# Kernel optimization log

Hardware: AMD Instinct MI355X
Metric: run time of the kernel (lower is better)

## Reference

```python
import jax, jax.numpy as jnp
import numpy as np

N_NODES = 100000
N_EDGES = 1600000
F_IN, F_HID, F_OUT = 48, 16, 16
K = 2  # kernel_size, dim=1, degree=1 open B-spline -> basis (1-u, u)


def glorot(key, shape):
    fan_in, fan_out = shape[-2], shape[-1]
    s = jnp.sqrt(6.0 / (fan_in + fan_out))
    return jax.random.uniform(key, shape, jnp.float32, -s, s)


def setup_inputs() -> dict:
    key = jax.random.key(0)
    ks = jax.random.split(key, 10)
    x = jax.random.normal(ks[0], (N_NODES, F_IN), jnp.float32)
    edge_attr = jax.random.uniform(ks[1], (N_EDGES, 1), jnp.float32)
    edge_index = jax.random.randint(ks[2], (2, N_EDGES), 0, N_NODES, jnp.int64)
    W1 = glorot(ks[3], (K, F_IN, F_HID))
    root1 = glorot(ks[4], (F_IN, F_HID))
    b1 = jnp.zeros((F_HID,), jnp.float32)
    W2 = glorot(ks[5], (K, F_HID, F_OUT))
    root2 = glorot(ks[6], (F_HID, F_OUT))
    b2 = jnp.zeros((F_OUT,), jnp.float32)
    return {"x": x, "edge_attr": edge_attr, "edge_index": edge_index,
            "W1": W1, "root1": root1, "b1": b1, "W2": W2, "root2": root2, "b2": b2}


def spline_conv(x, edge_index, u, W, root, bias, num_nodes):
    # x: [N,Fin], u: [E] pseudo coords in [0,1], W: [2,Fin,Fout]
    src, dst = edge_index[0], edge_index[1]
    xj = x[src]                                        # [E,Fin] gather
    m = jnp.einsum('ef,kfo->eko', xj, W)               # [E,2,Fout]
    basis = jnp.stack([1.0 - u, u], axis=1)            # linear open B-spline, K=2
    msg = jnp.einsum('ek,eko->eo', basis, m)           # [E,Fout]
    agg = jax.ops.segment_sum(msg, dst, num_segments=num_nodes)
    cnt = jax.ops.segment_sum(jnp.ones_like(msg[:, 0]), dst, num_segments=num_nodes)
    agg = agg / jnp.maximum(cnt, 1.0)[:, None]         # aggr='mean'
    return agg + x @ root + bias                       # root_weight + bias


def reference(x, edge_attr, edge_index, W1, root1, b1, W2, root2, b2):
    u = edge_attr[:, 0]
    h = jax.nn.elu(spline_conv(x, edge_index, u, W1, root1, b1, N_NODES))
    out = spline_conv(h, edge_index, u, W2, root2, b2, N_NODES)
    return jax.nn.log_softmax(out, axis=1)
```

## Files before the change

kernel.cpp:

```cpp
#include <hip/hip_runtime.h>
#include <math.h>

#define N_NODES 100000
#define N_EDGES 1600000
#define KC 8
#define KSH 3
#define NBUK 391
#define NCHUNK 256
#define CPE 6250
#define M_CNT (NBUK * NCHUNK)
#define SCB 512
#define NSC ((M_CNT + SCB - 1) / SCB)

__device__ __forceinline__ unsigned bf16_rne(float x) {
    unsigned u = __float_as_uint(x);
    return (u + 0x7FFFu + ((u >> 16) & 1u)) >> 16;
}

__device__ __forceinline__ void acc4(float* acc, uint4 w, float uu) {
    acc[0] += fmaf(uu, __uint_as_float(w.x & 0xFFFF0000u), __uint_as_float(w.x << 16));
    acc[1] += fmaf(uu, __uint_as_float(w.y & 0xFFFF0000u), __uint_as_float(w.y << 16));
    acc[2] += fmaf(uu, __uint_as_float(w.z & 0xFFFF0000u), __uint_as_float(w.z << 16));
    acc[3] += fmaf(uu, __uint_as_float(w.w & 0xFFFF0000u), __uint_as_float(w.w << 16));
}

__device__ __forceinline__ void edge_accum(unsigned pk,
                                           const uint4* __restrict__ YPH,
                                           float acc[16]) {
    float uu = (float)(pk >> 17) * (1.0f / 32767.0f);
    const uint4* yp = YPH + (size_t)(pk & 0x1FFFFu) * 4;
    uint4 w0 = yp[0], w1 = yp[1], w2 = yp[2], w3 = yp[3];
    acc4(acc + 0, w0, uu);
    acc4(acc + 4, w1, uu);
    acc4(acc + 8, w2, uu);
    acc4(acc + 12, w3, uu);
}

__device__ __forceinline__ void edge_accum2(unsigned p0, unsigned p1,
                                            const uint4* __restrict__ YPH,
                                            float acc[16]) {
    float u0 = (float)(p0 >> 17) * (1.0f / 32767.0f);
    float u1 = (float)(p1 >> 17) * (1.0f / 32767.0f);
    const uint4* a = YPH + (size_t)(p0 & 0x1FFFFu) * 4;
    const uint4* b = YPH + (size_t)(p1 & 0x1FFFFu) * 4;
    uint4 w0 = a[0], w1 = a[1], w2 = a[2], w3 = a[3];
    uint4 v0 = b[0], v1 = b[1], v2 = b[2], v3 = b[3];
    acc4(acc + 0, w0, u0);
    acc4(acc + 4, w1, u0);
    acc4(acc + 8, w2, u0);
    acc4(acc + 12, w3, u0);
    acc4(acc + 0, v0, u1);
    acc4(acc + 4, v1, u1);
    acc4(acc + 8, v2, u1);
    acc4(acc + 12, v3, u1);
}

__global__ __launch_bounds__(1024)
void fused_hist_transform(const float* __restrict__ X,
                          const float* __restrict__ W,
                          const float* __restrict__ root,
                          const float* __restrict__ bias,
                          unsigned* __restrict__ YPH, float* __restrict__ R,
                          const int* __restrict__ dst,
                          int* __restrict__ counts) {
    int t = threadIdx.x;
    if (blockIdx.x < NCHUNK) {
        __shared__ int h[NBUK];
        for (int i = t; i < NBUK; i += 1024) h[i] = 0;
        __syncthreads();
        int c = blockIdx.x;
        const int* dp = dst + c * CPE;
        for (int j = t; j < CPE; j += 1024) atomicAdd(&h[dp[j] >> 8], 1);
        __syncthreads();
        for (int i = t; i < NBUK; i += 1024) counts[i * NCHUNK + c] = h[i];
    } else {
        __shared__ float sW0[48 * 16];
        __shared__ float sWd[48 * 16];
        __shared__ float sR[48 * 16];
        __shared__ float sB[16];
        int bid = blockIdx.x - NCHUNK;
        for (int i = t; i < 48 * 16; i += 1024) {
            float w0 = W[i];
            float w1 = W[48 * 16 + i];
            sW0[i] = w0;
            sWd[i] = w1 - w0;
            sR[i]  = root[i];
        }
        if (t < 16) sB[t] = bias[t];
        __syncthreads();

        int idx = bid * 1024 + t;
        int n = idx >> 4;
        int o = idx & 15;
        if (n >= N_NODES) return;

        const float* xr = X + (long)n * 48;
        float a0 = 0.0f, a1 = 0.0f, ar = 0.0f;
        for (int f = 0; f < 48; ++f) {
            float xv = xr[f];
            a0 = fmaf(xv, sW0[f * 16 + o], a0);
            a1 = fmaf(xv, sWd[f * 16 + o], a1);
            ar = fmaf(xv, sR[f * 16 + o], ar);
        }
        YPH[idx] = bf16_rne(a0) | (bf16_rne(a1) << 16);
        R[idx]   = ar + sB[o];
    }
}

__global__ __launch_bounds__(SCB)
void scan_blocksum(const int* __restrict__ a, int* __restrict__ bsum) {
    __shared__ int s[SCB];
    int t = threadIdx.x;
    int i = blockIdx.x * SCB + t;
    s[t] = (i < M_CNT) ? a[i] : 0;
    __syncthreads();
    for (int off = SCB / 2; off > 0; off >>= 1) {
        if (t < off) s[t] += s[t + off];
        __syncthreads();
    }
    if (t == 0) bsum[blockIdx.x] = s[0];
}

__global__ __launch_bounds__(256)
void scan_bsum(int* __restrict__ bsum) {
    __shared__ int s[256];
    int t = threadIdx.x;
    int v = (t < NSC) ? bsum[t] : 0;
    s[t] = v;
    __syncthreads();
    for (int off = 1; off < 256; off <<= 1) {
        int x = (t >= off) ? s[t - off] : 0;
        __syncthreads();
        s[t] += x;
        __syncthreads();
    }
    if (t < NSC) bsum[t] = s[t] - v;
}

__global__ __launch_bounds__(SCB)
void scan_write(int* __restrict__ a, const int* __restrict__ bsum) {
    __shared__ int s[SCB];
    int t = threadIdx.x;
    int i = blockIdx.x * SCB + t;
    int v = (i < M_CNT) ? a[i] : 0;
    s[t] = v;
    __syncthreads();
    for (int off = 1; off < SCB; off <<= 1) {
        int x = (t >= off) ? s[t - off] : 0;
        __syncthreads();
        s[t] += x;
        __syncthreads();
    }
    if (i < M_CNT) a[i] = bsum[blockIdx.x] + s[t] - v;
}

__global__ __launch_bounds__(1024)
void scatter_edges(const int* __restrict__ src, const int* __restrict__ dst,
                   const float* __restrict__ u,
                   const int* __restrict__ offsets,
                   unsigned* __restrict__ pk, unsigned char* __restrict__ dl) {
    __shared__ unsigned upk[CPE];
    __shared__ unsigned short ubuk[CPE];
    __shared__ unsigned char udl[CPE];
    __shared__ unsigned spk[CPE];
    __shared__ unsigned char sdl[CPE];
    __shared__ int ls[NBUK + 1];
    __shared__ int lcur[NBUK];
    __shared__ int gbase[NBUK];
    __shared__ int sc[SCB];

    int t = threadIdx.x, c = blockIdx.x;

    for (int i = t; i < NBUK; i += 1024) lcur[i] = 0;
    __syncthreads();
    for (int j = t; j < CPE; j += 1024) {
        int e = c * CPE + j;
        int d = dst[e];
        float uu = u[e];
        uu = uu < 0.0f ? 0.0f : (uu > 1.0f ? 1.0f : uu);
        int u15 = (int)fmaf(uu, 32767.0f, 0.5f);
        upk[j] = (unsigned)src[e] | ((unsigned)u15 << 17);
        udl[j] = (unsigned char)(d & 255);
        int b = d >> 8;
        ubuk[j] = (unsigned short)b;
        atomicAdd(&lcur[b], 1);
    }
    __syncthreads();

    int v = 0;
    if (t < SCB) {
        v = (t < NBUK) ? lcur[t] : 0;
        sc[t] = v;
    }
    __syncthreads();
    for (int off = 1; off < SCB; off <<= 1) {
        int x = 0;
        if (t < SCB && t >= off) x = sc[t - off];
        __syncthreads();
        if (t < SCB) sc[t] += x;
        __syncthreads();
    }
    if (t < NBUK) {
        int ex = sc[t] - v;
        ls[t] = ex;
        lcur[t] = ex;
        gbase[t] = offsets[t * NCHUNK + c] - ex;
    }
    if (t == 0) ls[NBUK] = CPE;
    __syncthreads();

    for (int j = t; j < CPE; j += 1024) {
        int b = ubuk[j];
        int p = atomicAdd(&lcur[b], 1);
        spk[p] = upk[j];
        sdl[p] = udl[j];
    }
    __syncthreads();

    for (int j = t; j < CPE; j += 1024) {
        int lo = 0, hi = NBUK;
        while (hi - lo > 1) {
            int mid = (lo + hi) >> 1;
            if (ls[mid] <= j) lo = mid; else hi = mid;
        }
        int g = gbase[lo] + j;
        pk[g] = spk[j];
        dl[g] = sdl[j];
    }
}

__global__ __launch_bounds__(256)
void group_edges(const int* __restrict__ offsets,
                 const unsigned* __restrict__ pk_in,
                 const unsigned char* __restrict__ dl,
                 unsigned* __restrict__ pk_out,
                 int* __restrict__ rowptr) {
    __shared__ int h[256];
    __shared__ int pre[256];
    int b = blockIdx.x, t = threadIdx.x;
    int beg = offsets[b * NCHUNK];
    int end = (b + 1 < NBUK) ? offsets[(b + 1) * NCHUNK] : N_EDGES;
    h[t] = 0;
    __syncthreads();
    for (int j = beg + t; j < end; j += 256) atomicAdd(&h[dl[j]], 1);
    __syncthreads();
    int cntv = h[t];
    pre[t] = cntv;
    __syncthreads();
    for (int off = 1; off < 256; off <<= 1) {
        int x = (t >= off) ? pre[t - off] : 0;
        __syncthreads();
        pre[t] += x;
        __syncthreads();
    }
    int ex = pre[t] - cntv;
    int node0 = b << 8;
    if (node0 + t < N_NODES) rowptr[node0 + t] = beg + ex;
    if (b == 0 && t == 0) rowptr[N_NODES] = N_EDGES;
    __syncthreads();
    h[t] = ex;
    __syncthreads();
    for (int j = beg + t; j < end; j += 256) {
        int loc = dl[j];
        int pos = atomicAdd(&h[loc], 1);
        pk_out[beg + pos] = pk_in[j];
    }
}

__global__ __launch_bounds__(256)
void aggregate_elu_transform(const int* __restrict__ rowptr,
                             const unsigned* __restrict__ csr,
                             const uint4* __restrict__ YPH1,
                             const float* __restrict__ R1,
                             const float* __restrict__ W2,
                             const float* __restrict__ root2,
                             const float* __restrict__ b2,
                             unsigned* __restrict__ YPH2,
                             float* __restrict__ R2) {
    __shared__ float sW0[16 * 16];
    __shared__ float sWd[16 * 16];
    __shared__ float sR[16 * 16];
    __shared__ float sB[16];
    int t = threadIdx.x;
    {
        float w0 = W2[t];
        float w1 = W2[256 + t];
        sW0[t] = w0;
        sWd[t] = w1 - w0;
        sR[t]  = root2[t];
    }
    if (t < 16) sB[t] = b2[t];
    __syncthreads();

    int g = blockIdx.x * 256 + t;
    int n = g >> KSH;
    int h = g & (KC - 1);
    int beg = rowptr[n], end = rowptr[n + 1];
    int deg = end - beg;

    float acc[16];
#pragma unroll
    for (int i = 0; i < 16; ++i) acc[i] = 0.0f;
    int j = beg + h;
    for (; j + KC < end; j += 2 * KC) edge_accum2(csr[j], csr[j + KC], YPH1, acc);
    if (j < end) edge_accum(csr[j], YPH1, acc);

#pragma unroll
    for (int mask = 1; mask <= 4; mask <<= 1) {
#pragma unroll
        for (int i = 0; i < 16; ++i) acc[i] += __shfl_xor(acc[i], mask);
    }
    float inv = 1.0f / (deg > 0 ? (float)deg : 1.0f);

    float h16[16];
    const float4* rp = (const float4*)(R1 + (size_t)n * 16);
#pragma unroll
    for (int q = 0; q < 4; ++q) {
        float4 rr = rp[q];
        float v;
        v = fmaf(acc[4 * q + 0], inv, rr.x); h16[4 * q + 0] = v > 0.0f ? v : expm1f(v);
        v = fmaf(acc[4 * q + 1], inv, rr.y); h16[4 * q + 1] = v > 0.0f ? v : expm1f(v);
        v = fmaf(acc[4 * q + 2], inv, rr.z); h16[4 * q + 2] = v > 0.0f ? v : expm1f(v);
        v = fmaf(acc[4 * q + 3], inv, rr.w); h16[4 * q + 3] = v > 0.0f ? v : expm1f(v);
    }

    int o0 = 2 * h;
    float a0 = 0.0f, a1 = 0.0f, ar = 0.0f;
    float c0 = 0.0f, c1 = 0.0f, cr = 0.0f;
#pragma unroll
    for (int f = 0; f < 16; ++f) {
        float hv = h16[f];
        a0 = fmaf(hv, sW0[f * 16 + o0], a0);
        a1 = fmaf(hv, sWd[f * 16 + o0], a1);
        ar = fmaf(hv, sR[f * 16 + o0],  ar);
        c0 = fmaf(hv, sW0[f * 16 + o0 + 1], c0);
        c1 = fmaf(hv, sWd[f * 16 + o0 + 1], c1);
        cr = fmaf(hv, sR[f * 16 + o0 + 1],  cr);
    }
    ((uint2*)YPH2)[g] = make_uint2(bf16_rne(a0) | (bf16_rne(a1) << 16),
                                   bf16_rne(c0) | (bf16_rne(c1) << 16));
    ((float2*)R2)[g] = make_float2(ar + sB[o0], cr + sB[o0 + 1]);
}

__global__ __launch_bounds__(256)
void aggregate_logsoftmax(const int* __restrict__ rowptr,
                          const unsigned* __restrict__ csr,
                          const uint4* __restrict__ YPH,
                          const float* __restrict__ R,
                          float* __restrict__ out) {
    int g = blockIdx.x * 256 + threadIdx.x;
    int n = g >> KSH;
    int h = g & (KC - 1);
    int beg = rowptr[n], end = rowptr[n + 1];
    int deg = end - beg;

    float acc[16];
#pragma unroll
    for (int i = 0; i < 16; ++i) acc[i] = 0.0f;
    int j = beg + h;
    for (; j + KC < end; j += 2 * KC) edge_accum2(csr[j], csr[j + KC], YPH, acc);
    if (j < end) edge_accum(csr[j], YPH, acc);

#pragma unroll
    for (int mask = 1; mask <= 4; mask <<= 1) {
#pragma unroll
        for (int i = 0; i < 16; ++i) acc[i] += __shfl_xor(acc[i], mask);
    }
    float inv = 1.0f / (deg > 0 ? (float)deg : 1.0f);

    float2 rr = ((const float2*)R)[g];
    float v0 = fmaf(acc[2 * h + 0], inv, rr.x);
    float v1 = fmaf(acc[2 * h + 1], inv, rr.y);

    float m = fmaxf(v0, v1);
#pragma unroll
    for (int mask = 1; mask <= 4; mask <<= 1) m = fmaxf(m, __shfl_xor(m, mask));
    float s = expf(v0 - m) + expf(v1 - m);
#pragma unroll
    for (int mask = 1; mask <= 4; mask <<= 1) s += __shfl_xor(s, mask);
    float lse = m + logf(s);

    ((float2*)out)[g] = make_float2(v0 - lse, v1 - lse);
}

extern "C" void kernel_launch(void* const* d_in, const int* in_sizes, int n_in,
                              void* d_out, int out_size, void* d_ws, size_t ws_size,
                              hipStream_t stream) {
    const float* x         = (const float*)d_in[0];
    const float* edge_attr = (const float*)d_in[1];
    const int*   edge_idx  = (const int*)d_in[2];
    const float* W1        = (const float*)d_in[3];
    const float* root1     = (const float*)d_in[4];
    const float* b1        = (const float*)d_in[5];
    const float* W2        = (const float*)d_in[6];
    const float* root2     = (const float*)d_in[7];
    const float* b2        = (const float*)d_in[8];
    float* out = (float*)d_out;

    const int* src = edge_idx;
    const int* dst = edge_idx + N_EDGES;

    char* ws = (char*)d_ws;
    unsigned*      pk_in   = (unsigned*)(ws);
    unsigned*      pk_out  = (unsigned*)(ws + 6400000);
    unsigned char* dl      = (unsigned char*)(ws + 12800000);
    int*           counts  = (int*)(ws + 14400000);
    int*           rowptr  = (int*)(ws + 14800384);
    unsigned*      YPH1    = (unsigned*)(ws + 15200400);
    unsigned*      YPH2    = (unsigned*)(ws + 21600400);
    float*         R1      = (float*)(ws + 28000400);
    float*         R2      = (float*)(ws + 34400400);
    int*           bsum    = (int*)(ws + 40800400);

    dim3 gK1(NCHUNK + (N_NODES * 16 + 1023) / 1024);
    dim3 gAgg((N_NODES * KC) / 256);

    fused_hist_transform<<<gK1, 1024, 0, stream>>>(
        x, W1, root1, b1, YPH1, R1, dst, counts);
    scan_blocksum<<<NSC, SCB, 0, stream>>>(counts, bsum);
    scan_bsum<<<1, 256, 0, stream>>>(bsum);
    scan_write<<<NSC, SCB, 0, stream>>>(counts, bsum);
    scatter_edges<<<NCHUNK, 1024, 0, stream>>>(src, dst, edge_attr,
                                               counts, pk_in, dl);
    group_edges<<<NBUK, 256, 0, stream>>>(counts, pk_in, dl, pk_out, rowptr);

    aggregate_elu_transform<<<gAgg, 256, 0, stream>>>(
        rowptr, pk_out, (const uint4*)YPH1, R1, W2, root2, b2, YPH2, R2);

    aggregate_logsoftmax<<<gAgg, 256, 0, stream>>>(
        rowptr, pk_out, (const uint4*)YPH2, R2, out);
}
```

Baseline: 209.2 us.

## Replace global prefix scan with per-bucket totals and chunk-local edge runs

The three-kernel global scan over the bucket×chunk count matrix is replaced by one single-block kernel that sums each bucket's counts and scans the bucket totals. scatter_edges now writes each chunk's locally sorted edges contiguously into its own slice and records per-run local offsets, which removes the binary-search scattered global write. group_edges rebuilds run offsets per bucket and gathers from the 256 chunk runs via a binary search. This cuts two kernel launches and makes the scatter writes coalesced. In exchange, the single-block scan reads about 100K counts serially per thread, and group_edges reads its input more scattered and adds per-edge search cost.

```diff
diff --git a/kernel.cpp b/kernel.cpp
--- a/kernel.cpp
+++ b/kernel.cpp
@@ -8,9 +8,7 @@
 #define NBUK 391
 #define NCHUNK 256
 #define CPE 6250
-#define M_CNT (NBUK * NCHUNK)
 #define SCB 512
-#define NSC ((M_CNT + SCB - 1) / SCB)
 
 __device__ __forceinline__ unsigned bf16_rne(float x) {
     unsigned u = __float_as_uint(x);
@@ -108,42 +106,15 @@
 }
 
 __global__ __launch_bounds__(SCB)
-void scan_blocksum(const int* __restrict__ a, int* __restrict__ bsum) {
+void scan_buckets(const int* __restrict__ counts, int* __restrict__ bucket_base) {
     __shared__ int s[SCB];
     int t = threadIdx.x;
-    int i = blockIdx.x * SCB + t;
-    s[t] = (i < M_CNT) ? a[i] : 0;
-    __syncthreads();
-    for (int off = SCB / 2; off > 0; off >>= 1) {
-        if (t < off) s[t] += s[t + off];
-        __syncthreads();
-    }
-    if (t == 0) bsum[blockIdx.x] = s[0];
-}
-
-__global__ __launch_bounds__(256)
-void scan_bsum(int* __restrict__ bsum) {
-    __shared__ int s[256];
-    int t = threadIdx.x;
-    int v = (t < NSC) ? bsum[t] : 0;
-    s[t] = v;
-    __syncthreads();
-    for (int off = 1; off < 256; off <<= 1) {
-        int x = (t >= off) ? s[t - off] : 0;
-        __syncthreads();
-        s[t] += x;
-        __syncthreads();
-    }
-    if (t < NSC) bsum[t] = s[t] - v;
-}
-
-__global__ __launch_bounds__(SCB)
-void scan_write(int* __restrict__ a, const int* __restrict__ bsum) {
-    __shared__ int s[SCB];
-    int t = threadIdx.x;
-    int i = blockIdx.x * SCB + t;
-    int v = (i < M_CNT) ? a[i] : 0;
-    s[t] = v;
+    int tot = 0;
+    if (t < NBUK) {
+        const int* p = counts + t * NCHUNK;
+        for (int cc = 0; cc < NCHUNK; ++cc) tot += p[cc];
+    }
+    s[t] = tot;
     __syncthreads();
     for (int off = 1; off < SCB; off <<= 1) {
         int x = (t >= off) ? s[t - off] : 0;
@@ -151,22 +122,21 @@
         s[t] += x;
         __syncthreads();
     }
-    if (i < M_CNT) a[i] = bsum[blockIdx.x] + s[t] - v;
+    if (t < NBUK) bucket_base[t] = s[t] - tot;
+    if (t == 0) bucket_base[NBUK] = N_EDGES;
 }
 
 __global__ __launch_bounds__(1024)
 void scatter_edges(const int* __restrict__ src, const int* __restrict__ dst,
                    const float* __restrict__ u,
-                   const int* __restrict__ offsets,
-                   unsigned* __restrict__ pk, unsigned char* __restrict__ dl) {
+                   unsigned* __restrict__ pk, unsigned char* __restrict__ dl,
+                   int* __restrict__ run_ls) {
     __shared__ unsigned upk[CPE];
     __shared__ unsigned short ubuk[CPE];
     __shared__ unsigned char udl[CPE];
     __shared__ unsigned spk[CPE];
     __shared__ unsigned char sdl[CPE];
-    __shared__ int ls[NBUK + 1];
     __shared__ int lcur[NBUK];
-    __shared__ int gbase[NBUK];
     __shared__ int sc[SCB];
 
     int t = threadIdx.x, c = blockIdx.x;
@@ -202,11 +172,9 @@
     }
     if (t < NBUK) {
         int ex = sc[t] - v;
-        ls[t] = ex;
         lcur[t] = ex;
-        gbase[t] = offsets[t * NCHUNK + c] - ex;
-    }
-    if (t == 0) ls[NBUK] = CPE;
+        run_ls[t * NCHUNK + c] = ex;
+    }
     __syncthreads();
 
     for (int j = t; j < CPE; j += 1024) {
@@ -217,32 +185,52 @@
     }
     __syncthreads();
 
+    unsigned* po = pk + (size_t)c * CPE;
+    unsigned char* dlo = dl + (size_t)c * CPE;
     for (int j = t; j < CPE; j += 1024) {
-        int lo = 0, hi = NBUK;
-        while (hi - lo > 1) {
-            int mid = (lo + hi) >> 1;
-            if (ls[mid] <= j) lo = mid; else hi = mid;
-        }
-        int g = gbase[lo] + j;
-        pk[g] = spk[j];
-        dl[g] = sdl[j];
+        po[j] = spk[j];
+        dlo[j] = sdl[j];
     }
 }
 
 __global__ __launch_bounds__(256)
-void group_edges(const int* __restrict__ offsets,
+void group_edges(const int* __restrict__ counts, const int* __restrict__ run_ls,
                  const unsigned* __restrict__ pk_in,
-                 const unsigned char* __restrict__ dl,
-                 unsigned* __restrict__ pk_out,
-                 int* __restrict__ rowptr) {
+                 const unsigned char* __restrict__ dl_in,
+                 const int* __restrict__ bucket_base,
+                 unsigned* __restrict__ pk_out, int* __restrict__ rowptr) {
+    __shared__ int rcnt[NCHUNK];
+    __shared__ int roff[NCHUNK + 1];
+    __shared__ int rls[NCHUNK];
     __shared__ int h[256];
     __shared__ int pre[256];
     int b = blockIdx.x, t = threadIdx.x;
-    int beg = offsets[b * NCHUNK];
-    int end = (b + 1 < NBUK) ? offsets[(b + 1) * NCHUNK] : N_EDGES;
+
+    rcnt[t] = counts[b * NCHUNK + t];
+    rls[t]  = run_ls[b * NCHUNK + t];
     h[t] = 0;
-    __syncthreads();
-    for (int j = beg + t; j < end; j += 256) atomicAdd(&h[dl[j]], 1);
+    pre[t] = rcnt[t];
+    __syncthreads();
+    for (int off = 1; off < 256; off <<= 1) {
+        int x = (t >= off) ? pre[t - off] : 0;
+        __syncthreads();
+        pre[t] += x;
+        __syncthreads();
+    }
+    roff[t] = pre[t] - rcnt[t];
+    if (t == 255) roff[256] = pre[255];
+    __syncthreads();
+    int tot = roff[256];
+
+    for (int j = t; j < tot; j += 256) {
+        int lo = 0, hi = NCHUNK;
+        while (hi - lo > 1) {
+            int mid = (lo + hi) >> 1;
+            if (roff[mid] <= j) lo = mid; else hi = mid;
+        }
+        int idx = lo * CPE + rls[lo] + (j - roff[lo]);
+        atomicAdd(&h[dl_in[idx]], 1);
+    }
     __syncthreads();
     int cntv = h[t];
     pre[t] = cntv;
@@ -255,15 +243,23 @@
     }
     int ex = pre[t] - cntv;
     int node0 = b << 8;
-    if (node0 + t < N_NODES) rowptr[node0 + t] = beg + ex;
+    int base = bucket_base[b];
+    if (node0 + t < N_NODES) rowptr[node0 + t] = base + ex;
     if (b == 0 && t == 0) rowptr[N_NODES] = N_EDGES;
     __syncthreads();
     h[t] = ex;
     __syncthreads();
-    for (int j = beg + t; j < end; j += 256) {
-        int loc = dl[j];
+
+    for (int j = t; j < tot; j += 256) {
+        int lo = 0, hi = NCHUNK;
+        while (hi - lo > 1) {
+            int mid = (lo + hi) >> 1;
+            if (roff[mid] <= j) lo = mid; else hi = mid;
+        }
+        int idx = lo * CPE + rls[lo] + (j - roff[lo]);
+        int loc = dl_in[idx];
         int pos = atomicAdd(&h[loc], 1);
-        pk_out[beg + pos] = pk_in[j];
+        pk_out[base + pos] = pk_in[idx];
     }
 }
 
@@ -405,24 +401,24 @@
     unsigned*      pk_out  = (unsigned*)(ws + 6400000);
     unsigned char* dl      = (unsigned char*)(ws + 12800000);
     int*           counts  = (int*)(ws + 14400000);
-    int*           rowptr  = (int*)(ws + 14800384);
-    unsigned*      YPH1    = (unsigned*)(ws + 15200400);
-    unsigned*      YPH2    = (unsigned*)(ws + 21600400);
-    float*         R1      = (float*)(ws + 28000400);
-    float*         R2      = (float*)(ws + 34400400);
-    int*           bsum    = (int*)(ws + 40800400);
+    int*           run_ls  = (int*)(ws + 14800384);
+    int*           rowptr  = (int*)(ws + 15200768);
+    int*           bbase   = (int*)(ws + 15600784);
+    unsigned*      YPH1    = (unsigned*)(ws + 15602400);
+    unsigned*      YPH2    = (unsigned*)(ws + 22002400);
+    float*         R1      = (float*)(ws + 28402400);
+    float*         R2      = (float*)(ws + 34802400);
 
     dim3 gK1(NCHUNK + (N_NODES * 16 + 1023) / 1024);
     dim3 gAgg((N_NODES * KC) / 256);
 
     fused_hist_transform<<<gK1, 1024, 0, stream>>>(
         x, W1, root1, b1, YPH1, R1, dst, counts);
-    scan_blocksum<<<NSC, SCB, 0, stream>>>(counts, bsum);
-    scan_bsum<<<1, 256, 0, stream>>>(bsum);
-    scan_write<<<NSC, SCB, 0, stream>>>(counts, bsum);
+    scan_buckets<<<1, SCB, 0, stream>>>(counts, bbase);
     scatter_edges<<<NCHUNK, 1024, 0, stream>>>(src, dst, edge_attr,
-                                               counts, pk_in, dl);
-    group_edges<<<NBUK, 256, 0, stream>>>(counts, pk_in, dl, pk_out, rowptr);
+                                               pk_in, dl, run_ls);
+    group_edges<<<NBUK, 256, 0, stream>>>(counts, run_ls, pk_in, dl,
+                                          bbase, pk_out, rowptr);
 
     aggregate_elu_transform<<<gAgg, 256, 0, stream>>>(
         rowptr, pk_out, (const uint4*)YPH1, R1, W2, root2, b2, YPH2, R2);
```

Result: slower. 227.3 us (+8.7%).

## Split aggregation by feature slice per lane instead of by edge

Applied to the files above, without the earlier changes.

Each of the 8 lanes per node now walks every edge of the node but loads only its own 2-feature slice (8 bytes) of the bf16 message row, instead of striding over edges and loading full 64-byte rows. This removes the 16-value cross-lane shuffle reduction, and in the first layer the hidden vector is rebuilt with 16 broadcasts. The 8 lanes now read consecutive 8-byte pieces of the same row, so the gathers coalesce. The cost is that every lane redundantly reads each csr entry and runs a loop as long as the full node degree, which lengthens the dependent-load chain per thread.

```diff
diff --git a/kernel.cpp b/kernel.cpp
--- a/kernel.cpp
+++ b/kernel.cpp
@@ -15,44 +15,6 @@
 __device__ __forceinline__ unsigned bf16_rne(float x) {
     unsigned u = __float_as_uint(x);
     return (u + 0x7FFFu + ((u >> 16) & 1u)) >> 16;
-}
-
-__device__ __forceinline__ void acc4(float* acc, uint4 w, float uu) {
-    acc[0] += fmaf(uu, __uint_as_float(w.x & 0xFFFF0000u), __uint_as_float(w.x << 16));
-    acc[1] += fmaf(uu, __uint_as_float(w.y & 0xFFFF0000u), __uint_as_float(w.y << 16));
-    acc[2] += fmaf(uu, __uint_as_float(w.z & 0xFFFF0000u), __uint_as_float(w.z << 16));
-    acc[3] += fmaf(uu, __uint_as_float(w.w & 0xFFFF0000u), __uint_as_float(w.w << 16));
-}
-
-__device__ __forceinline__ void edge_accum(unsigned pk,
-                                           const uint4* __restrict__ YPH,
-                                           float acc[16]) {
-    float uu = (float)(pk >> 17) * (1.0f / 32767.0f);
-    const uint4* yp = YPH + (size_t)(pk & 0x1FFFFu) * 4;
-    uint4 w0 = yp[0], w1 = yp[1], w2 = yp[2], w3 = yp[3];
-    acc4(acc + 0, w0, uu);
-    acc4(acc + 4, w1, uu);
-    acc4(acc + 8, w2, uu);
-    acc4(acc + 12, w3, uu);
-}
-
-__device__ __forceinline__ void edge_accum2(unsigned p0, unsigned p1,
-                                            const uint4* __restrict__ YPH,
-                                            float acc[16]) {
-    float u0 = (float)(p0 >> 17) * (1.0f / 32767.0f);
-    float u1 = (float)(p1 >> 17) * (1.0f / 32767.0f);
-    const uint4* a = YPH + (size_t)(p0 & 0x1FFFFu) * 4;
-    const uint4* b = YPH + (size_t)(p1 & 0x1FFFFu) * 4;
-    uint4 w0 = a[0], w1 = a[1], w2 = a[2], w3 = a[3];
-    uint4 v0 = b[0], v1 = b[1], v2 = b[2], v3 = b[3];
-    acc4(acc + 0, w0, u0);
-    acc4(acc + 4, w1, u0);
-    acc4(acc + 8, w2, u0);
-    acc4(acc + 12, w3, u0);
-    acc4(acc + 0, v0, u1);
-    acc4(acc + 4, v1, u1);
-    acc4(acc + 8, v2, u1);
-    acc4(acc + 12, v3, u1);
 }
 
 __global__ __launch_bounds__(1024)
@@ -267,10 +229,38 @@
     }
 }
 
+__device__ __forceinline__ void octet_accumulate(
+        int beg, int end, int h, const unsigned* __restrict__ csr,
+        const unsigned* __restrict__ YPH, float* a0, float* a1) {
+    float s0 = 0.0f, s1 = 0.0f;
+    int j = beg;
+    for (; j + 1 < end; j += 2) {
+        unsigned p0 = csr[j];
+        unsigned p1 = csr[j + 1];
+        uint2 w0 = *(const uint2*)(YPH + (size_t)(p0 & 0x1FFFFu) * 16 + 2 * h);
+        uint2 w1 = *(const uint2*)(YPH + (size_t)(p1 & 0x1FFFFu) * 16 + 2 * h);
+        float u0 = (float)(p0 >> 17) * (1.0f / 32767.0f);
+        float u1 = (float)(p1 >> 17) * (1.0f / 32767.0f);
+        s0 += fmaf(u0, __uint_as_float(w0.x & 0xFFFF0000u), __uint_as_float(w0.x << 16));
+        s1 += fmaf(u0, __uint_as_float(w0.y & 0xFFFF0000u), __uint_as_float(w0.y << 16));
+        s0 += fmaf(u1, __uint_as_float(w1.x & 0xFFFF0000u), __uint_as_float(w1.x << 16));
+        s1 += fmaf(u1, __uint_as_float(w1.y & 0xFFFF0000u), __uint_as_float(w1.y << 16));
+    }
+    if (j < end) {
+        unsigned p0 = csr[j];
+        uint2 w0 = *(const uint2*)(YPH + (size_t)(p0 & 0x1FFFFu) * 16 + 2 * h);
+        float u0 = (float)(p0 >> 17) * (1.0f / 32767.0f);
+        s0 += fmaf(u0, __uint_as_float(w0.x & 0xFFFF0000u), __uint_as_float(w0.x << 16));
+        s1 += fmaf(u0, __uint_as_float(w0.y & 0xFFFF0000u), __uint_as_float(w0.y << 16));
+    }
+    *a0 = s0;
+    *a1 = s1;
+}
+
 __global__ __launch_bounds__(256)
 void aggregate_elu_transform(const int* __restrict__ rowptr,
                              const unsigned* __restrict__ csr,
-                             const uint4* __restrict__ YPH1,
+                             const unsigned* __restrict__ YPH1,
                              const float* __restrict__ R1,
                              const float* __restrict__ W2,
                              const float* __restrict__ root2,
@@ -298,54 +288,46 @@
     int beg = rowptr[n], end = rowptr[n + 1];
     int deg = end - beg;
 
-    float acc[16];
+    float a0, a1;
+    octet_accumulate(beg, end, h, csr, YPH1, &a0, &a1);
+    float inv = 1.0f / (deg > 0 ? (float)deg : 1.0f);
+
+    float2 rr = ((const float2*)R1)[g];
+    float v0 = fmaf(a0, inv, rr.x);
+    float v1 = fmaf(a1, inv, rr.y);
+    v0 = v0 > 0.0f ? v0 : expm1f(v0);
+    v1 = v1 > 0.0f ? v1 : expm1f(v1);
+
+    int base = (t & 63) & ~7;
+    float h16[16];
 #pragma unroll
-    for (int i = 0; i < 16; ++i) acc[i] = 0.0f;
-    int j = beg + h;
-    for (; j + KC < end; j += 2 * KC) edge_accum2(csr[j], csr[j + KC], YPH1, acc);
-    if (j < end) edge_accum(csr[j], YPH1, acc);
-
-#pragma unroll
-    for (int mask = 1; mask <= 4; mask <<= 1) {
-#pragma unroll
-        for (int i = 0; i < 16; ++i) acc[i] += __shfl_xor(acc[i], mask);
-    }
-    float inv = 1.0f / (deg > 0 ? (float)deg : 1.0f);
-
-    float h16[16];
-    const float4* rp = (const float4*)(R1 + (size_t)n * 16);
-#pragma unroll
-    for (int q = 0; q < 4; ++q) {
-        float4 rr = rp[q];
-        float v;
-        v = fmaf(acc[4 * q + 0], inv, rr.x); h16[4 * q + 0] = v > 0.0f ? v : expm1f(v);
-        v = fmaf(acc[4 * q + 1], inv, rr.y); h16[4 * q + 1] = v > 0.0f ? v : expm1f(v);
-        v = fmaf(acc[4 * q + 2], inv, rr.z); h16[4 * q + 2] = v > 0.0f ? v : expm1f(v);
-        v = fmaf(acc[4 * q + 3], inv, rr.w); h16[4 * q + 3] = v > 0.0f ? v : expm1f(v);
+    for (int k = 0; k < 8; ++k) {
+        h16[2 * k + 0] = __shfl(v0, base + k, 64);
+        h16[2 * k + 1] = __shfl(v1, base + k, 64);
     }
 
     int o0 = 2 * h;
-    float a0 = 0.0f, a1 = 0.0f, ar = 0.0f;
-    float c0 = 0.0f, c1 = 0.0f, cr = 0.0f;
+    float y0 = 0.0f, y1 = 0.0f, yr = 0.0f;
+    float z0 = 0.0f, z1 = 0.0f, zr = 0.0f;
 #pragma unroll
     for (int f = 0; f < 16; ++f) {
         float hv = h16[f];
-        a0 = fmaf(hv, sW0[f * 16 + o0], a0);
-        a1 = fmaf(hv, sWd[f * 16 + o0], a1);
-        ar = fmaf(hv, sR[f * 16 + o0],  ar);
-        c0 = fmaf(hv, sW0[f * 16 + o0 + 1], c0);
-        c1 = fmaf(hv, sWd[f * 16 + o0 + 1], c1);
-        cr = fmaf(hv, sR[f * 16 + o0 + 1],  cr);
-    }
-    ((uint2*)YPH2)[g] = make_uint2(bf16_rne(a0) | (bf16_rne(a1) << 16),
-                                   bf16_rne(c0) | (bf16_rne(c1) << 16));
-    ((float2*)R2)[g] = make_float2(ar + sB[o0], cr + sB[o0 + 1]);
+        y0 = fmaf(hv, sW0[f * 16 + o0], y0);
+        y1 = fmaf(hv, sWd[f * 16 + o0], y1);
+        yr = fmaf(hv, sR[f * 16 + o0],  yr);
+        z0 = fmaf(hv, sW0[f * 16 + o0 + 1], z0);
+        z1 = fmaf(hv, sWd[f * 16 + o0 + 1], z1);
+        zr = fmaf(hv, sR[f * 16 + o0 + 1],  zr);
+    }
+    ((uint2*)YPH2)[g] = make_uint2(bf16_rne(y0) | (bf16_rne(y1) << 16),
+                                   bf16_rne(z0) | (bf16_rne(z1) << 16));
+    ((float2*)R2)[g] = make_float2(yr + sB[o0], zr + sB[o0 + 1]);
 }
 
 __global__ __launch_bounds__(256)
 void aggregate_logsoftmax(const int* __restrict__ rowptr,
                           const unsigned* __restrict__ csr,
-                          const uint4* __restrict__ YPH,
+                          const unsigned* __restrict__ YPH,
                           const float* __restrict__ R,
                           float* __restrict__ out) {
     int g = blockIdx.x * 256 + threadIdx.x;
@@ -354,23 +336,13 @@
     int beg = rowptr[n], end = rowptr[n + 1];
     int deg = end - beg;
 
-    float acc[16];
-#pragma unroll
-    for (int i = 0; i < 16; ++i) acc[i] = 0.0f;
-    int j = beg + h;
-    for (; j + KC < end; j += 2 * KC) edge_accum2(csr[j], csr[j + KC], YPH, acc);
-    if (j < end) edge_accum(csr[j], YPH, acc);
-
-#pragma unroll
-    for (int mask = 1; mask <= 4; mask <<= 1) {
-#pragma unroll
-        for (int i = 0; i < 16; ++i) acc[i] += __shfl_xor(acc[i], mask);
-    }
+    float a0, a1;
+    octet_accumulate(beg, end, h, csr, YPH, &a0, &a1);
     float inv = 1.0f / (deg > 0 ? (float)deg : 1.0f);
 
     float2 rr = ((const float2*)R)[g];
-    float v0 = fmaf(acc[2 * h + 0], inv, rr.x);
-    float v1 = fmaf(acc[2 * h + 1], inv, rr.y);
+    float v0 = fmaf(a0, inv, rr.x);
+    float v1 = fmaf(a1, inv, rr.y);
 
     float m = fmaxf(v0, v1);
 #pragma unroll
@@ -425,8 +397,8 @@
     group_edges<<<NBUK, 256, 0, stream>>>(counts, pk_in, dl, pk_out, rowptr);
 
     aggregate_elu_transform<<<gAgg, 256, 0, stream>>>(
-        rowptr, pk_out, (const uint4*)YPH1, R1, W2, root2, b2, YPH2, R2);
+        rowptr, pk_out, YPH1, R1, W2, root2, b2, YPH2, R2);
 
     aggregate_logsoftmax<<<gAgg, 256, 0, stream>>>(
-        rowptr, pk_out, (const uint4*)YPH2, R2, out);
-}
+        rowptr, pk_out, YPH2, R2, out);
+}
```

Result: slower. 216.9 us (+3.7%).
